# Kernel optimization log

Hardware: AMD Instinct MI355X
Metric: run time of the kernel (lower is better)

Reference implementation:

```python
import jax, jax.numpy as jnp
import numpy as np

N = 100000   # nodes
E = 1600000  # edges (avg degree 16)
F = 256      # in_channels
H = 4        # heads
C = 32       # out_channels per head
NEG_SLOPE = 0.2  # PyG GATConv default leaky_relu slope


def setup_inputs() -> dict:
    key = jax.random.key(0)
    k0, k1, k2, k3, k4 = jax.random.split(key, 5)
    x = jax.random.normal(k0, (N, F), dtype=jnp.float32)
    edge_index = jax.random.randint(k1, (2, E), 0, N, dtype=jnp.int32)
    W = jax.random.normal(k2, (F, H * C), dtype=jnp.float32) * 0.05
    att_src = jax.random.normal(k3, (H, C), dtype=jnp.float32) * 0.05
    att_dst = jax.random.normal(k4, (H, C), dtype=jnp.float32) * 0.05
    bias = jnp.zeros((H * C,), dtype=jnp.float32)
    return {"x": x, "edge_index": edge_index, "W": W,
            "att_src": att_src, "att_dst": att_dst, "bias": bias}


def reference(x, edge_index, W, att_src, att_dst, bias):
    n = x.shape[0]
    h_, c_ = att_src.shape
    # add self loops (PyG default add_self_loops=True)
    loops = jnp.arange(n, dtype=edge_index.dtype)
    src = jnp.concatenate([edge_index[0], loops])  # source node j of each edge
    dst = jnp.concatenate([edge_index[1], loops])  # target node i of each edge
    # linear projection, per-head view: [N, H, C]
    h = (x @ W).reshape(n, h_, c_)
    # per-node attention halves: [N, H]
    a_src = jnp.einsum('nhc,hc->nh', h, att_src)
    a_dst = jnp.einsum('nhc,hc->nh', h, att_dst)
    # per-edge logits with leaky relu: [Etot, H]
    e = jax.nn.leaky_relu(a_src[src] + a_dst[dst], NEG_SLOPE)
    # segment softmax over edges sharing the same destination
    m = jax.ops.segment_max(e, dst, num_segments=n)
    m = jnp.where(jnp.isfinite(m), m, jnp.zeros_like(m))  # isolated nodes
    p = jnp.exp(e - m[dst])
    s = jax.ops.segment_sum(p, dst, num_segments=n)
    alpha = p / (s[dst] + 1e-16)  # [Etot, H]
    # weighted scatter-aggregate of source features
    msg = h[src] * alpha[:, :, None]  # [Etot, H, C]
    out = jax.ops.segment_sum(msg, dst, num_segments=n)  # [N, H, C]
    return out.reshape(n, h_ * c_) + bias
```

## Files before the change

kernel.cpp:

```cpp
#include <hip/hip_runtime.h>

#define NEG_SLOPE 0.2f
#define CAP 64
#define NPART 8

typedef __attribute__((ext_vector_type(8))) short short8;
typedef __attribute__((ext_vector_type(4))) float f32x4;

__device__ __forceinline__ float lrelu(float x) {
    return x > 0.0f ? x : NEG_SLOPE * x;
}

__device__ __forceinline__ unsigned short f2bf(float f) {
    unsigned int u = __float_as_uint(f);
    u += 0x7FFFu + ((u >> 16) & 1u);
    return (unsigned short)(u >> 16);
}

__device__ __forceinline__ float2 bfpair(unsigned int u) {
    float2 r;
    r.x = __uint_as_float(u << 16);
    r.y = __uint_as_float(u & 0xFFFF0000u);
    return r;
}

__global__ void convW_kernel(const float* __restrict__ W, unsigned short* __restrict__ Wtf) {
    int idx = blockIdx.x * blockDim.x + threadIdx.x;
    int j = idx & 7;
    int lane = (idx >> 3) & 63;
    int f = idx >> 9;
    int t = f >> 3;
    int ks = f & 7;
    int k = ks * 32 + (lane >> 4) * 8 + j;
    int nn = t * 16 + (lane & 15);
    Wtf[idx] = f2bf(W[k * 128 + nn]);
}

__global__ __launch_bounds__(256) void gemm_fused_kernel(
    const float* __restrict__ x, const unsigned short* __restrict__ Wtf,
    const float* __restrict__ att_src, const float* __restrict__ att_dst,
    unsigned short* __restrict__ hb, float* __restrict__ a_src,
    float* __restrict__ a_dst, int n) {
    __shared__ unsigned short Bs[32768];
    int tid = threadIdx.x;

    #pragma unroll
    for (int it = 0; it < 16; ++it) {
        int o = (it * 256 + tid) * 8;
        *(short8*)&Bs[o] = *(const short8*)&Wtf[o];
    }
    __syncthreads();

    int wave = tid >> 6;
    int lane = tid & 63;
    int ln = lane & 15;
    int quad = lane >> 4;
    int row0w = blockIdx.x * 128 + wave * 32;

    int r0 = row0w + ln;       if (r0 >= n) r0 = n - 1;
    int r1 = row0w + 16 + ln;  if (r1 >= n) r1 = n - 1;
    const float* xr0 = &x[(size_t)r0 * 256];
    const float* xr1 = &x[(size_t)r1 * 256];

    f32x4 acc[2][8];
    #pragma unroll
    for (int rt = 0; rt < 2; ++rt)
        #pragma unroll
        for (int t = 0; t < 8; ++t) acc[rt][t] = (f32x4){0.f, 0.f, 0.f, 0.f};

    #pragma unroll
    for (int ks = 0; ks < 8; ++ks) {
        int ko = ks * 32 + quad * 8;
        float4 a00 = *(const float4*)&xr0[ko];
        float4 a01 = *(const float4*)&xr0[ko + 4];
        float4 a10 = *(const float4*)&xr1[ko];
        float4 a11 = *(const float4*)&xr1[ko + 4];
        short8 af0, af1;
        af0[0] = (short)f2bf(a00.x); af0[1] = (short)f2bf(a00.y);
        af0[2] = (short)f2bf(a00.z); af0[3] = (short)f2bf(a00.w);
        af0[4] = (short)f2bf(a01.x); af0[5] = (short)f2bf(a01.y);
        af0[6] = (short)f2bf(a01.z); af0[7] = (short)f2bf(a01.w);
        af1[0] = (short)f2bf(a10.x); af1[1] = (short)f2bf(a10.y);
        af1[2] = (short)f2bf(a10.z); af1[3] = (short)f2bf(a10.w);
        af1[4] = (short)f2bf(a11.x); af1[5] = (short)f2bf(a11.y);
        af1[6] = (short)f2bf(a11.z); af1[7] = (short)f2bf(a11.w);
        #pragma unroll
        for (int t = 0; t < 8; ++t) {
            short8 bf = *(const short8*)&Bs[(((t * 8 + ks) * 64) + lane) * 8];
            acc[0][t] = __builtin_amdgcn_mfma_f32_16x16x32_bf16(af0, bf, acc[0][t], 0, 0, 0);
            acc[1][t] = __builtin_amdgcn_mfma_f32_16x16x32_bf16(af1, bf, acc[1][t], 0, 0, 0);
        }
    }

    #pragma unroll
    for (int rt = 0; rt < 2; ++rt) {
        #pragma unroll
        for (int t = 0; t < 8; ++t) {
            #pragma unroll
            for (int r = 0; r < 4; ++r) {
                int grow = row0w + rt * 16 + quad * 4 + r;
                if (grow < n) hb[(size_t)grow * 128 + t * 16 + ln] = f2bf(acc[rt][t][r]);
            }
        }
    }

    #pragma unroll
    for (int hd = 0; hd < 4; ++hd) {
        float as1 = att_src[hd * 32 + ln];
        float as2 = att_src[hd * 32 + 16 + ln];
        float ad1 = att_dst[hd * 32 + ln];
        float ad2 = att_dst[hd * 32 + 16 + ln];
        #pragma unroll
        for (int rt = 0; rt < 2; ++rt) {
            #pragma unroll
            for (int r = 0; r < 4; ++r) {
                float ps = acc[rt][2 * hd][r] * as1 + acc[rt][2 * hd + 1][r] * as2;
                float pd = acc[rt][2 * hd][r] * ad1 + acc[rt][2 * hd + 1][r] * ad2;
                #pragma unroll
                for (int off = 1; off < 16; off <<= 1) {
                    ps += __shfl_xor(ps, off);
                    pd += __shfl_xor(pd, off);
                }
                if (ln == 0) {
                    int grow = row0w + rt * 16 + quad * 4 + r;
                    if (grow < n) {
                        a_src[grow * 4 + hd] = ps;
                        a_dst[grow * 4 + hd] = pd;
                    }
                }
            }
        }
    }
}

__global__ __launch_bounds__(256) void build_kernel(
    const int* __restrict__ src, const int* __restrict__ dst,
    int* __restrict__ deg, int* __restrict__ bucket, int e, int n) {
    int p = blockIdx.x & (NPART - 1);
    int slice = blockIdx.x >> 3;
    int nslices = gridDim.x >> 3;
    int part = (n + NPART - 1) / NPART;
    unsigned lo = (unsigned)(p * part);
    int e4 = e >> 2;
    int stride = nslices * 256;
    const int4* dst4 = (const int4*)dst;
    const int4* src4 = (const int4*)src;
    for (int i = slice * 256 + threadIdx.x; i < e4; i += stride) {
        int4 d4 = dst4[i];
        int4 s4 = src4[i];
        if ((unsigned)(d4.x - lo) < (unsigned)part) {
            int r = atomicAdd(&deg[d4.x], 1);
            if (r < CAP) bucket[d4.x * CAP + r] = s4.x;
        }
        if ((unsigned)(d4.y - lo) < (unsigned)part) {
            int r = atomicAdd(&deg[d4.y], 1);
            if (r < CAP) bucket[d4.y * CAP + r] = s4.y;
        }
        if ((unsigned)(d4.z - lo) < (unsigned)part) {
            int r = atomicAdd(&deg[d4.z], 1);
            if (r < CAP) bucket[d4.z * CAP + r] = s4.z;
        }
        if ((unsigned)(d4.w - lo) < (unsigned)part) {
            int r = atomicAdd(&deg[d4.w], 1);
            if (r < CAP) bucket[d4.w * CAP + r] = s4.w;
        }
    }
    if (blockIdx.x == 0 && threadIdx.x < (e & 3)) {
        int i = e4 * 4 + threadIdx.x;
        int d = dst[i];
        int r = atomicAdd(&deg[d], 1);
        if (r < CAP) bucket[d * CAP + r] = src[i];
    }
}

__global__ __launch_bounds__(256) void aggregate_kernel(
    const unsigned short* __restrict__ hb, const float* __restrict__ a_src,
    const float* __restrict__ a_dst, const int* __restrict__ deg,
    const int* __restrict__ bucket, const float* __restrict__ bias,
    float* __restrict__ out, int n) {
    __shared__ float lds_alpha[4][CAP][4];
    __shared__ int lds_s[4][CAP];
    int wave = threadIdx.x >> 6;
    int lane = threadIdx.x & 63;
    int node = blockIdx.x * 4 + wave;
    if (node >= n) node = n - 1;
    int el = lane & 15;
    int hh = lane >> 4;

    int cnt = deg[node];
    if (cnt > CAP) cnt = CAP;

    float adst = a_dst[node * 4 + hh];
    float e_self = lrelu(a_src[node * 4 + hh] + adst);

    float e_gp[4];
    int s_gp[4];
    float mloc = e_self;
    #pragma unroll
    for (int g = 0; g < 4; ++g) {
        int p = g * 16 + el;
        if (p < cnt) {
            int s = bucket[(unsigned)node * CAP + p];
            s_gp[g] = s;
            float ev = lrelu(a_src[s * 4 + hh] + adst);
            e_gp[g] = ev;
            mloc = fmaxf(mloc, ev);
        } else {
            s_gp[g] = node;
            e_gp[g] = -INFINITY;
        }
    }
    #pragma unroll
    for (int off = 1; off < 16; off <<= 1)
        mloc = fmaxf(mloc, __shfl_xor(mloc, off));

    float pe_gp[4];
    float dloc = 0.0f;
    #pragma unroll
    for (int g = 0; g < 4; ++g) {
        float pe = __expf(e_gp[g] - mloc);
        pe_gp[g] = pe;
        dloc += pe;
    }
    #pragma unroll
    for (int off = 1; off < 16; off <<= 1)
        dloc += __shfl_xor(dloc, off);

    float pe_self = __expf(e_self - mloc);
    float inv = 1.0f / (dloc + pe_self);
    float alpha_self = pe_self * inv;

    #pragma unroll
    for (int g = 0; g < 4; ++g) {
        lds_alpha[wave][g * 16 + el][hh] = pe_gp[g] * inv;
        if (hh == 0) lds_s[wave][g * 16 + el] = s_gp[g];
    }
    __syncthreads();

    const unsigned int* hbu = (const unsigned int*)hb;
    float2 acc;
    {
        float2 hv = bfpair(hbu[(unsigned)node * 64u + lane]);
        acc.x = alpha_self * hv.x;
        acc.y = alpha_self * hv.y;
    }
    int p = 0;
    for (; p + 8 <= cnt; p += 8) {
        int4 sA = *(const int4*)&lds_s[wave][p];
        int4 sB = *(const int4*)&lds_s[wave][p + 4];
        unsigned int v0 = hbu[(unsigned)sA.x * 64u + lane];
        unsigned int v1 = hbu[(unsigned)sA.y * 64u + lane];
        unsigned int v2 = hbu[(unsigned)sA.z * 64u + lane];
        unsigned int v3 = hbu[(unsigned)sA.w * 64u + lane];
        unsigned int v4 = hbu[(unsigned)sB.x * 64u + lane];
        unsigned int v5 = hbu[(unsigned)sB.y * 64u + lane];
        unsigned int v6 = hbu[(unsigned)sB.z * 64u + lane];
        unsigned int v7 = hbu[(unsigned)sB.w * 64u + lane];
        float al0 = lds_alpha[wave][p + 0][hh];
        float al1 = lds_alpha[wave][p + 1][hh];
        float al2 = lds_alpha[wave][p + 2][hh];
        float al3 = lds_alpha[wave][p + 3][hh];
        float al4 = lds_alpha[wave][p + 4][hh];
        float al5 = lds_alpha[wave][p + 5][hh];
        float al6 = lds_alpha[wave][p + 6][hh];
        float al7 = lds_alpha[wave][p + 7][hh];
        float2 h0 = bfpair(v0), h1 = bfpair(v1), h2 = bfpair(v2), h3 = bfpair(v3);
        float2 h4 = bfpair(v4), h5 = bfpair(v5), h6 = bfpair(v6), h7 = bfpair(v7);
        acc.x += al0 * h0.x + al1 * h1.x + al2 * h2.x + al3 * h3.x
               + al4 * h4.x + al5 * h5.x + al6 * h6.x + al7 * h7.x;
        acc.y += al0 * h0.y + al1 * h1.y + al2 * h2.y + al3 * h3.y
               + al4 * h4.y + al5 * h5.y + al6 * h6.y + al7 * h7.y;
    }
    for (; p + 4 <= cnt; p += 4) {
        int4 sA = *(const int4*)&lds_s[wave][p];
        unsigned int v0 = hbu[(unsigned)sA.x * 64u + lane];
        unsigned int v1 = hbu[(unsigned)sA.y * 64u + lane];
        unsigned int v2 = hbu[(unsigned)sA.z * 64u + lane];
        unsigned int v3 = hbu[(unsigned)sA.w * 64u + lane];
        float al0 = lds_alpha[wave][p + 0][hh];
        float al1 = lds_alpha[wave][p + 1][hh];
        float al2 = lds_alpha[wave][p + 2][hh];
        float al3 = lds_alpha[wave][p + 3][hh];
        float2 h0 = bfpair(v0), h1 = bfpair(v1), h2 = bfpair(v2), h3 = bfpair(v3);
        acc.x += al0 * h0.x + al1 * h1.x + al2 * h2.x + al3 * h3.x;
        acc.y += al0 * h0.y + al1 * h1.y + al2 * h2.y + al3 * h3.y;
    }
    for (; p < cnt; ++p) {
        int s = lds_s[wave][p];
        float al = lds_alpha[wave][p][hh];
        float2 hv = bfpair(hbu[(unsigned)s * 64u + lane]);
        acc.x += al * hv.x;
        acc.y += al * hv.y;
    }

    int oc = hh * 32 + el * 2;
    float2 b2 = *(const float2*)&bias[oc];
    float2 o;
    o.x = acc.x + b2.x;
    o.y = acc.y + b2.y;
    *(float2*)&out[(size_t)node * 128 + oc] = o;
}

extern "C" void kernel_launch(void* const* d_in, const int* in_sizes, int n_in,
                              void* d_out, int out_size, void* d_ws, size_t ws_size,
                              hipStream_t stream) {
    const float* x = (const float*)d_in[0];
    const int* edge_index = (const int*)d_in[1];
    const float* W = (const float*)d_in[2];
    const float* att_src = (const float*)d_in[3];
    const float* att_dst = (const float*)d_in[4];
    const float* bias = (const float*)d_in[5];
    float* out = (float*)d_out;

    int n = in_sizes[0] / 256;
    int e = in_sizes[1] / 2;
    const int* esrc = edge_index;
    const int* edst = edge_index + e;

    char* w = (char*)d_ws;
    unsigned short* hb = (unsigned short*)w;  w += (size_t)n * 128 * 2;
    float* a_src = (float*)w;                 w += (size_t)n * 4 * 4;
    float* a_dst = (float*)w;                 w += (size_t)n * 4 * 4;
    unsigned short* Wtf = (unsigned short*)w; w += 128 * 256 * 2;
    int* deg = (int*)w;                       w += (size_t)n * 4;
    int* bucket = (int*)w;                    w += (size_t)n * CAP * 4;

    hipMemsetAsync(deg, 0, (size_t)n * sizeof(int), stream);

    convW_kernel<<<128, 256, 0, stream>>>(W, Wtf);
    gemm_fused_kernel<<<(n + 127) / 128, 256, 0, stream>>>(x, Wtf, att_src, att_dst,
                                                           hb, a_src, a_dst, n);
    build_kernel<<<256 * NPART, 256, 0, stream>>>(esrc, edst, deg, bucket, e, n);
    aggregate_kernel<<<(n + 3) / 4, 256, 0, stream>>>(hb, a_src, a_dst, deg,
                                                      bucket, bias, out, n);
}
```

Measured before the change: 355.6 us.

## Merge W conversion, GEMM and CSR build into one interleaved front kernel

Drops the separate W-to-bf16 conversion kernel: each GEMM block now converts W straight into LDS. The GEMM and bucket-build kernels become one launch whose blocks alternate between GEMM and edge-bucketing roles, so compute-bound and atomic-bound work can run side by side and two launches go away. The build now uses 128 slice groups instead of 256, and every GEMM block repeats the strided W conversion, which adds redundant global reads.

```diff
diff --git a/kernel.cpp b/kernel.cpp
--- a/kernel.cpp
+++ b/kernel.cpp
@@ -3,6 +3,7 @@
 #define NEG_SLOPE 0.2f
 #define CAP 64
 #define NPART 8
+#define BUILD_GROUPS 128
 
 typedef __attribute__((ext_vector_type(8))) short short8;
 typedef __attribute__((ext_vector_type(4))) float f32x4;
@@ -24,30 +25,78 @@
     return r;
 }
 
-__global__ void convW_kernel(const float* __restrict__ W, unsigned short* __restrict__ Wtf) {
-    int idx = blockIdx.x * blockDim.x + threadIdx.x;
-    int j = idx & 7;
-    int lane = (idx >> 3) & 63;
-    int f = idx >> 9;
-    int t = f >> 3;
-    int ks = f & 7;
-    int k = ks * 32 + (lane >> 4) * 8 + j;
-    int nn = t * 16 + (lane & 15);
-    Wtf[idx] = f2bf(W[k * 128 + nn]);
-}
-
-__global__ __launch_bounds__(256) void gemm_fused_kernel(
-    const float* __restrict__ x, const unsigned short* __restrict__ Wtf,
+__global__ __launch_bounds__(256) void front_kernel(
+    const float* __restrict__ x, const float* __restrict__ W,
     const float* __restrict__ att_src, const float* __restrict__ att_dst,
+    const int* __restrict__ esrc, const int* __restrict__ edst,
+    int* __restrict__ deg, int* __restrict__ bucket,
     unsigned short* __restrict__ hb, float* __restrict__ a_src,
-    float* __restrict__ a_dst, int n) {
+    float* __restrict__ a_dst, int n, int e, int gg) {
     __shared__ unsigned short Bs[32768];
     int tid = threadIdx.x;
+    int g = blockIdx.x >> 3;
+    int lg = blockIdx.x & 7;
+    bool isGemm;
+    int idx;
+    if (g < 2 * gg) {
+        isGemm = ((g & 1) == 0);
+        idx = (g >> 1) * 8 + lg;
+    } else {
+        isGemm = false;
+        idx = gg * 8 + (g - 2 * gg) * 8 + lg;
+    }
+
+    if (!isGemm) {
+        int p = idx & 7;
+        int slice = idx >> 3;
+        int part = (n + NPART - 1) / NPART;
+        unsigned lo = (unsigned)(p * part);
+        int e4 = e >> 2;
+        int stride = BUILD_GROUPS * 256;
+        const int4* dst4 = (const int4*)edst;
+        const int4* src4 = (const int4*)esrc;
+        for (int i = slice * 256 + tid; i < e4; i += stride) {
+            int4 d4 = dst4[i];
+            int4 s4 = src4[i];
+            if ((unsigned)(d4.x - lo) < (unsigned)part) {
+                int r = atomicAdd(&deg[d4.x], 1);
+                if (r < CAP) bucket[d4.x * CAP + r] = s4.x;
+            }
+            if ((unsigned)(d4.y - lo) < (unsigned)part) {
+                int r = atomicAdd(&deg[d4.y], 1);
+                if (r < CAP) bucket[d4.y * CAP + r] = s4.y;
+            }
+            if ((unsigned)(d4.z - lo) < (unsigned)part) {
+                int r = atomicAdd(&deg[d4.z], 1);
+                if (r < CAP) bucket[d4.z * CAP + r] = s4.z;
+            }
+            if ((unsigned)(d4.w - lo) < (unsigned)part) {
+                int r = atomicAdd(&deg[d4.w], 1);
+                if (r < CAP) bucket[d4.w * CAP + r] = s4.w;
+            }
+        }
+        if (idx == 0 && tid < (e & 3)) {
+            int i = e4 * 4 + tid;
+            int d = edst[i];
+            int r = atomicAdd(&deg[d], 1);
+            if (r < CAP) bucket[d * CAP + r] = esrc[i];
+        }
+        return;
+    }
 
     #pragma unroll
     for (int it = 0; it < 16; ++it) {
-        int o = (it * 256 + tid) * 8;
-        *(short8*)&Bs[o] = *(const short8*)&Wtf[o];
+        int base = it * 256 + tid;
+        int lane_ = base & 63;
+        int f = base >> 6;
+        int t = f >> 3;
+        int ks = f & 7;
+        int nn = t * 16 + (lane_ & 15);
+        const float* wp = &W[(ks * 32 + ((lane_ >> 4)) * 8) * 128 + nn];
+        short8 bfv;
+        #pragma unroll
+        for (int j = 0; j < 8; ++j) bfv[j] = (short)f2bf(wp[j * 128]);
+        *(short8*)&Bs[base * 8] = bfv;
     }
     __syncthreads();
 
@@ -55,7 +104,7 @@
     int lane = tid & 63;
     int ln = lane & 15;
     int quad = lane >> 4;
-    int row0w = blockIdx.x * 128 + wave * 32;
+    int row0w = idx * 128 + wave * 32;
 
     int r0 = row0w + ln;       if (r0 >= n) r0 = n - 1;
     int r1 = row0w + 16 + ln;  if (r1 >= n) r1 = n - 1;
@@ -130,46 +179,6 @@
                 }
             }
         }
-    }
-}
-
-__global__ __launch_bounds__(256) void build_kernel(
-    const int* __restrict__ src, const int* __restrict__ dst,
-    int* __restrict__ deg, int* __restrict__ bucket, int e, int n) {
-    int p = blockIdx.x & (NPART - 1);
-    int slice = blockIdx.x >> 3;
-    int nslices = gridDim.x >> 3;
-    int part = (n + NPART - 1) / NPART;
-    unsigned lo = (unsigned)(p * part);
-    int e4 = e >> 2;
-    int stride = nslices * 256;
-    const int4* dst4 = (const int4*)dst;
-    const int4* src4 = (const int4*)src;
-    for (int i = slice * 256 + threadIdx.x; i < e4; i += stride) {
-        int4 d4 = dst4[i];
-        int4 s4 = src4[i];
-        if ((unsigned)(d4.x - lo) < (unsigned)part) {
-            int r = atomicAdd(&deg[d4.x], 1);
-            if (r < CAP) bucket[d4.x * CAP + r] = s4.x;
-        }
-        if ((unsigned)(d4.y - lo) < (unsigned)part) {
-            int r = atomicAdd(&deg[d4.y], 1);
-            if (r < CAP) bucket[d4.y * CAP + r] = s4.y;
-        }
-        if ((unsigned)(d4.z - lo) < (unsigned)part) {
-            int r = atomicAdd(&deg[d4.z], 1);
-            if (r < CAP) bucket[d4.z * CAP + r] = s4.z;
-        }
-        if ((unsigned)(d4.w - lo) < (unsigned)part) {
-            int r = atomicAdd(&deg[d4.w], 1);
-            if (r < CAP) bucket[d4.w * CAP + r] = s4.w;
-        }
-    }
-    if (blockIdx.x == 0 && threadIdx.x < (e & 3)) {
-        int i = e4 * 4 + threadIdx.x;
-        int d = dst[i];
-        int r = atomicAdd(&deg[d], 1);
-        if (r < CAP) bucket[d * CAP + r] = src[i];
     }
 }
 
@@ -321,16 +330,17 @@
     unsigned short* hb = (unsigned short*)w;  w += (size_t)n * 128 * 2;
     float* a_src = (float*)w;                 w += (size_t)n * 4 * 4;
     float* a_dst = (float*)w;                 w += (size_t)n * 4 * 4;
-    unsigned short* Wtf = (unsigned short*)w; w += 128 * 256 * 2;
     int* deg = (int*)w;                       w += (size_t)n * 4;
     int* bucket = (int*)w;                    w += (size_t)n * CAP * 4;
 
     hipMemsetAsync(deg, 0, (size_t)n * sizeof(int), stream);
 
-    convW_kernel<<<128, 256, 0, stream>>>(W, Wtf);
-    gemm_fused_kernel<<<(n + 127) / 128, 256, 0, stream>>>(x, Wtf, att_src, att_dst,
-                                                           hb, a_src, a_dst, n);
-    build_kernel<<<256 * NPART, 256, 0, stream>>>(esrc, edst, deg, bucket, e, n);
+    int ngb = (n + 127) / 128;
+    int gg = (ngb + 7) / 8;
+    int grid = (gg + BUILD_GROUPS) * 8;
+    front_kernel<<<grid, 256, 0, stream>>>(x, W, att_src, att_dst, esrc, edst,
+                                           deg, bucket, hb, a_src, a_dst,
+                                           n, e, gg);
     aggregate_kernel<<<(n + 3) / 4, 256, 0, stream>>>(hb, a_src, a_dst, deg,
                                                       bucket, bias, out, n);
 }
```

Result: slower. 369.1 us (+3.8%).

## Pre-convert x to bf16 MFMA fragment layout in a separate pass

Applied to the files above, without the earlier changes.

Adds a conversion kernel that turns x into bf16 laid out in MFMA fragment order, and converts W in the same launch using packed v_cvt_pk_bf16_f32. The GEMM then loads pre-swizzled bf16 fragments straight from global memory and reads W from global instead of staging it in LDS, removing the LDS fill and barrier. The intent is cheaper, vectorized A-operand loads and less conversion ALU work inside the GEMM. The cost is an extra full pass over x: an fp32 read plus a bf16 write and read back, about 100 MB of additional traffic. The build kernel is also reordered to run before the GEMM.

```diff
diff --git a/kernel.cpp b/kernel.cpp
--- a/kernel.cpp
+++ b/kernel.cpp
@@ -15,6 +15,12 @@
     unsigned int u = __float_as_uint(f);
     u += 0x7FFFu + ((u >> 16) & 1u);
     return (unsigned short)(u >> 16);
+}
+
+__device__ __forceinline__ unsigned int cvtpk(float lo, float hi) {
+    unsigned int r;
+    asm("v_cvt_pk_bf16_f32 %0, %1, %2" : "=v"(r) : "v"(lo), "v"(hi));
+    return r;
 }
 
 __device__ __forceinline__ float2 bfpair(unsigned int u) {
@@ -24,43 +30,64 @@
     return r;
 }
 
-__global__ void convW_kernel(const float* __restrict__ W, unsigned short* __restrict__ Wtf) {
-    int idx = blockIdx.x * blockDim.x + threadIdx.x;
-    int j = idx & 7;
-    int lane = (idx >> 3) & 63;
-    int f = idx >> 9;
-    int t = f >> 3;
-    int ks = f & 7;
-    int k = ks * 32 + (lane >> 4) * 8 + j;
-    int nn = t * 16 + (lane & 15);
-    Wtf[idx] = f2bf(W[k * 128 + nn]);
+__global__ __launch_bounds__(256) void conv_kernel(
+    const float* __restrict__ x, const float* __restrict__ W,
+    unsigned short* __restrict__ xbf, unsigned short* __restrict__ Wtf,
+    int n, int ntiles) {
+    int u = blockIdx.x * 256 + threadIdx.x;
+    int Tx = ntiles * 512;
+    if (u < Tx) {
+        int lane = u & 63;
+        int ks = (u >> 6) & 7;
+        int tile = u >> 9;
+        int row = tile * 16 + (lane & 15);
+        if (row >= n) row = n - 1;
+        int k0 = ks * 32 + (lane >> 4) * 8;
+        const float* xp = &x[(size_t)row * 256 + k0];
+        float4 a = *(const float4*)xp;
+        float4 b = *(const float4*)(xp + 4);
+        uint4 o;
+        o.x = cvtpk(a.x, a.y);
+        o.y = cvtpk(a.z, a.w);
+        o.z = cvtpk(b.x, b.y);
+        o.w = cvtpk(b.z, b.w);
+        *(uint4*)&xbf[(size_t)u * 8] = o;
+    } else if (u < Tx + 4096) {
+        int v = u - Tx;
+        int lane = v & 63;
+        int f = v >> 6;
+        int t = f >> 3;
+        int ks = f & 7;
+        int nn = t * 16 + (lane & 15);
+        int kb = ks * 32 + (lane >> 4) * 8;
+        const float* wp = &W[(size_t)kb * 128 + nn];
+        float w0 = wp[0 * 128], w1 = wp[1 * 128], w2 = wp[2 * 128], w3 = wp[3 * 128];
+        float w4 = wp[4 * 128], w5 = wp[5 * 128], w6 = wp[6 * 128], w7 = wp[7 * 128];
+        uint4 o;
+        o.x = cvtpk(w0, w1);
+        o.y = cvtpk(w2, w3);
+        o.z = cvtpk(w4, w5);
+        o.w = cvtpk(w6, w7);
+        *(uint4*)&Wtf[v * 8] = o;
+    }
 }
 
 __global__ __launch_bounds__(256) void gemm_fused_kernel(
-    const float* __restrict__ x, const unsigned short* __restrict__ Wtf,
+    const unsigned short* __restrict__ xbf, const unsigned short* __restrict__ Wtf,
     const float* __restrict__ att_src, const float* __restrict__ att_dst,
     unsigned short* __restrict__ hb, float* __restrict__ a_src,
-    float* __restrict__ a_dst, int n) {
-    __shared__ unsigned short Bs[32768];
+    float* __restrict__ a_dst, int n, int ntiles) {
     int tid = threadIdx.x;
-
-    #pragma unroll
-    for (int it = 0; it < 16; ++it) {
-        int o = (it * 256 + tid) * 8;
-        *(short8*)&Bs[o] = *(const short8*)&Wtf[o];
-    }
-    __syncthreads();
-
     int wave = tid >> 6;
     int lane = tid & 63;
     int ln = lane & 15;
     int quad = lane >> 4;
     int row0w = blockIdx.x * 128 + wave * 32;
 
-    int r0 = row0w + ln;       if (r0 >= n) r0 = n - 1;
-    int r1 = row0w + 16 + ln;  if (r1 >= n) r1 = n - 1;
-    const float* xr0 = &x[(size_t)r0 * 256];
-    const float* xr1 = &x[(size_t)r1 * 256];
+    int t0 = blockIdx.x * 8 + wave * 2;
+    int t1 = t0 + 1;
+    if (t0 >= ntiles) t0 = ntiles - 1;
+    if (t1 >= ntiles) t1 = ntiles - 1;
 
     f32x4 acc[2][8];
     #pragma unroll
@@ -70,23 +97,11 @@
 
     #pragma unroll
     for (int ks = 0; ks < 8; ++ks) {
-        int ko = ks * 32 + quad * 8;
-        float4 a00 = *(const float4*)&xr0[ko];
-        float4 a01 = *(const float4*)&xr0[ko + 4];
-        float4 a10 = *(const float4*)&xr1[ko];
-        float4 a11 = *(const float4*)&xr1[ko + 4];
-        short8 af0, af1;
-        af0[0] = (short)f2bf(a00.x); af0[1] = (short)f2bf(a00.y);
-        af0[2] = (short)f2bf(a00.z); af0[3] = (short)f2bf(a00.w);
-        af0[4] = (short)f2bf(a01.x); af0[5] = (short)f2bf(a01.y);
-        af0[6] = (short)f2bf(a01.z); af0[7] = (short)f2bf(a01.w);
-        af1[0] = (short)f2bf(a10.x); af1[1] = (short)f2bf(a10.y);
-        af1[2] = (short)f2bf(a10.z); af1[3] = (short)f2bf(a10.w);
-        af1[4] = (short)f2bf(a11.x); af1[5] = (short)f2bf(a11.y);
-        af1[6] = (short)f2bf(a11.z); af1[7] = (short)f2bf(a11.w);
+        short8 af0 = *(const short8*)&xbf[(size_t)((t0 * 8 + ks) * 64 + lane) * 8];
+        short8 af1 = *(const short8*)&xbf[(size_t)((t1 * 8 + ks) * 64 + lane) * 8];
         #pragma unroll
         for (int t = 0; t < 8; ++t) {
-            short8 bf = *(const short8*)&Bs[(((t * 8 + ks) * 64) + lane) * 8];
+            short8 bf = *(const short8*)&Wtf[(size_t)(((t * 8 + ks) * 64) + lane) * 8];
             acc[0][t] = __builtin_amdgcn_mfma_f32_16x16x32_bf16(af0, bf, acc[0][t], 0, 0, 0);
             acc[1][t] = __builtin_amdgcn_mfma_f32_16x16x32_bf16(af1, bf, acc[1][t], 0, 0, 0);
         }
@@ -316,6 +331,7 @@
     int e = in_sizes[1] / 2;
     const int* esrc = edge_index;
     const int* edst = edge_index + e;
+    int ntiles = (n + 15) / 16;
 
     char* w = (char*)d_ws;
     unsigned short* hb = (unsigned short*)w;  w += (size_t)n * 128 * 2;
@@ -324,13 +340,15 @@
     unsigned short* Wtf = (unsigned short*)w; w += 128 * 256 * 2;
     int* deg = (int*)w;                       w += (size_t)n * 4;
     int* bucket = (int*)w;                    w += (size_t)n * CAP * 4;
+    unsigned short* xbf = (unsigned short*)w; w += (size_t)ntiles * 512 * 8 * 2;
 
     hipMemsetAsync(deg, 0, (size_t)n * sizeof(int), stream);
 
-    convW_kernel<<<128, 256, 0, stream>>>(W, Wtf);
-    gemm_fused_kernel<<<(n + 127) / 128, 256, 0, stream>>>(x, Wtf, att_src, att_dst,
-                                                           hb, a_src, a_dst, n);
+    int Tx = ntiles * 512;
+    conv_kernel<<<(Tx + 4096 + 255) / 256, 256, 0, stream>>>(x, W, xbf, Wtf, n, ntiles);
     build_kernel<<<256 * NPART, 256, 0, stream>>>(esrc, edst, deg, bucket, e, n);
+    gemm_fused_kernel<<<(n + 127) / 128, 256, 0, stream>>>(xbf, Wtf, att_src, att_dst,
+                                                           hb, a_src, a_dst, n, ntiles);
     aggregate_kernel<<<(n + 3) / 4, 256, 0, stream>>>(hb, a_src, a_dst, deg,
                                                       bucket, bias, out, n);
 }
```

Result: slower. 381.7 us (+7.4%).
